# Kernel optimization log

Measured on AMD Instinct MI355X. Metric: run time of the kernel, lower is better.

## Reference

```python
import jax, jax.numpy as jnp
import numpy as np

EPS = 1e-5

def setup_inputs() -> dict:
    key = jax.random.key(0)
    k1, k2 = jax.random.split(key)
    x = jax.random.normal(k1, (4, 2048, 4096), dtype=jnp.float32)
    weight = jax.random.normal(k2, (4096, 4096), dtype=jnp.float32)
    return {"x": x, "weight": weight}

def reference(x, weight):
    # Weight quantization: ternary via absmean scaling.
    delta = jnp.mean(jnp.abs(weight)) + EPS
    w_quant = jnp.clip(jnp.round(weight / delta), -1.0, 1.0)
    w_final = w_quant * delta  # dequantized ternary weights

    # Activation quantization: int8 via per-row absmax.
    gamma = jnp.max(jnp.abs(x), axis=-1, keepdims=True) + EPS
    x_quant = jnp.clip(jnp.round(127.0 * x / gamma), -128.0, 127.0)
    x_quant = (gamma / 127.0) * x_quant
    # NOTE: original forward divides the dequantized activations by gamma
    # again (x_final = x_quant / gamma) -> effectively rounded / 127.
    x_final = x_quant / gamma

    # F.linear(x, W) = x @ W.T
    return jnp.einsum('bsi,oi->bso', x_final, w_final)
```

## Files before the change

### kernel.cpp

```cpp
#include <hip/hip_runtime.h>

#define EPS 1e-5f

typedef int int32x4 __attribute__((ext_vector_type(4)));

typedef const __attribute__((address_space(1))) unsigned int* gaddr_t;
typedef __attribute__((address_space(3))) unsigned int* laddr_t;


__global__ __launch_bounds__(256) void k_abssum(const float* __restrict__ w,
                                                double* __restrict__ partials) {
    int t = threadIdx.x;
    const float4* wv = (const float4*)w + (size_t)blockIdx.x * 4096;
    double s = 0.0;
#pragma unroll
    for (int i = 0; i < 16; ++i) {
        float4 v = wv[i * 256 + t];
        s += (double)(fabsf(v.x) + fabsf(v.y) + fabsf(v.z) + fabsf(v.w));
    }
    for (int off = 32; off; off >>= 1) s += __shfl_down(s, off);
    __shared__ double sm[4];
    int lane = t & 63, wid = t >> 6;
    if (lane == 0) sm[wid] = s;
    __syncthreads();
    if (t == 0) partials[blockIdx.x] = sm[0] + sm[1] + sm[2] + sm[3];
}

__global__ __launch_bounds__(256) void k_delta(const double* __restrict__ partials,
                                               float* __restrict__ delta) {
    int t = threadIdx.x;
    double s = partials[t] + partials[t + 256] + partials[t + 512] + partials[t + 768];
    for (int off = 32; off; off >>= 1) s += __shfl_down(s, off);
    __shared__ double sm[4];
    int lane = t & 63, wid = t >> 6;
    if (lane == 0) sm[wid] = s;
    __syncthreads();
    if (t == 0) {
        double mean = (sm[0] + sm[1] + sm[2] + sm[3]) / 16777216.0;
        *delta = (float)mean + EPS;
    }
}


__global__ __launch_bounds__(256) void k_wquant(const float* __restrict__ w,
                                                const float* __restrict__ deltap,
                                                signed char* __restrict__ tq) {
    float delta = *deltap;
    int t = threadIdx.x;
    size_t b4 = (size_t)blockIdx.x * 4096;
    const float4* wv = (const float4*)w;
    int* qo = (int*)tq;
#pragma unroll
    for (int i = 0; i < 16; ++i) {
        float4 v = wv[b4 + i * 256 + t];
        float a[4] = {v.x, v.y, v.z, v.w};
        int packed = 0;
#pragma unroll
        for (int j = 0; j < 4; ++j) {
            float r = rintf(a[j] / delta);
            r = fminf(1.0f, fmaxf(-1.0f, r));
            packed |= ((int)r & 0xff) << (8 * j);
        }
        qo[b4 + i * 256 + t] = packed;
    }
}

__global__ __launch_bounds__(256) void k_xquant(const float* __restrict__ x,
                                                signed char* __restrict__ q) {
    int t = threadIdx.x;
    size_t rbase = (size_t)blockIdx.x * 4096;
    const float4* xv = (const float4*)(x + rbase);
    float4 v[4];
    float m = 0.0f;
#pragma unroll
    for (int i = 0; i < 4; ++i) {
        v[i] = xv[i * 256 + t];
        m = fmaxf(m, fmaxf(fmaxf(fabsf(v[i].x), fabsf(v[i].y)),
                           fmaxf(fabsf(v[i].z), fabsf(v[i].w))));
    }
    for (int off = 32; off; off >>= 1) m = fmaxf(m, __shfl_xor(m, off));
    __shared__ float wm[4];
    int lane = t & 63, wid = t >> 6;
    if (lane == 0) wm[wid] = m;
    __syncthreads();
    float gamma = fmaxf(fmaxf(wm[0], wm[1]), fmaxf(wm[2], wm[3])) + EPS;
    int* qo = (int*)(q + rbase);
#pragma unroll
    for (int i = 0; i < 4; ++i) {
        float a[4] = {v[i].x, v[i].y, v[i].z, v[i].w};
        int packed = 0;
#pragma unroll
        for (int j = 0; j < 4; ++j) {
            float r = rintf(127.0f * a[j] / gamma);
            r = fminf(127.0f, fmaxf(-128.0f, r));
            packed |= ((int)r & 0xff) << (8 * j);
        }
        qo[i * 256 + t] = packed;
    }
}

__global__ __launch_bounds__(256) void k_gemm(const signed char* __restrict__ A,
                                              const signed char* __restrict__ B,
                                              const float* __restrict__ deltap,
                                              float* __restrict__ C) {
    __shared__ alignas(16) signed char As[8192];
    __shared__ alignas(16) signed char Bs[8192];

    int t = threadIdx.x;
    int lane = t & 63, wid = t >> 6;
    int wr = wid >> 1, wc = wid & 1;

    size_t brow = (size_t)blockIdx.y * 128;
    size_t bcol = (size_t)blockIdx.x * 128;

    int32x4 acc[4][4];
#pragma unroll
    for (int i = 0; i < 4; ++i)
#pragma unroll
        for (int j = 0; j < 4; ++j) acc[i][j] = (int32x4)(0);

    const signed char* ga = A + (brow + (size_t)(wid * 16 + (lane >> 2))) * 4096 + (lane & 3) * 16;
    const signed char* gb = B + (bcol + (size_t)(wid * 16 + (lane >> 2))) * 4096 + (lane & 3) * 16;
    signed char* lA = As + wid * 1024;
    signed char* lB = Bs + wid * 1024;

    int fa_off = (wr * 64 + (lane & 15)) * 64 + (lane >> 4) * 16;
    int fb_off = (wc * 64 + (lane & 15)) * 64 + (lane >> 4) * 16;

    for (int kt = 0; kt < 64; ++kt) {
        int koff = kt * 64;
        __builtin_amdgcn_global_load_lds((gaddr_t)(ga + koff), (laddr_t)lA, 16, 0, 0);
        __builtin_amdgcn_global_load_lds((gaddr_t)(ga + koff + (size_t)64 * 4096),
                                         (laddr_t)(lA + 4096), 16, 0, 0);
        __builtin_amdgcn_global_load_lds((gaddr_t)(gb + koff), (laddr_t)lB, 16, 0, 0);
        __builtin_amdgcn_global_load_lds((gaddr_t)(gb + koff + (size_t)64 * 4096),
                                         (laddr_t)(lB + 4096), 16, 0, 0);
        __syncthreads();

        int32x4 af[4], bf[4];
#pragma unroll
        for (int i = 0; i < 4; ++i)
            af[i] = *(const int32x4*)(As + fa_off + i * 16 * 64);
#pragma unroll
        for (int j = 0; j < 4; ++j)
            bf[j] = *(const int32x4*)(Bs + fb_off + j * 16 * 64);

#pragma unroll
        for (int i = 0; i < 4; ++i)
#pragma unroll
            for (int j = 0; j < 4; ++j)
                acc[i][j] = __builtin_amdgcn_mfma_i32_16x16x64_i8(af[i], bf[j], acc[i][j], 0, 0, 0);
        __syncthreads();
    }

    float scale = (*deltap) / 127.0f;
    size_t orow0 = brow + wr * 64 + (lane >> 4) * 4;
    size_t ocol0 = bcol + wc * 64 + (lane & 15);
#pragma unroll
    for (int i = 0; i < 4; ++i)
#pragma unroll
        for (int j = 0; j < 4; ++j) {
#pragma unroll
            for (int r = 0; r < 4; ++r) {
                C[(orow0 + i * 16 + r) * 4096 + ocol0 + j * 16] =
                    scale * (float)acc[i][j][r];
            }
        }
}


__global__ __launch_bounds__(256) void k_gamma(const float* __restrict__ x,
                                               float* __restrict__ gamma) {
    int t = threadIdx.x;
    size_t rbase = (size_t)blockIdx.x * 4096;
    const float4* xv = (const float4*)(x + rbase);
    float m = 0.0f;
#pragma unroll
    for (int i = 0; i < 4; ++i) {
        float4 v = xv[i * 256 + t];
        m = fmaxf(m, fmaxf(fmaxf(fabsf(v.x), fabsf(v.y)),
                           fmaxf(fabsf(v.z), fabsf(v.w))));
    }
    for (int off = 32; off; off >>= 1) m = fmaxf(m, __shfl_xor(m, off));
    __shared__ float wm[4];
    int lane = t & 63, wid = t >> 6;
    if (lane == 0) wm[wid] = m;
    __syncthreads();
    if (t == 0) gamma[blockIdx.x] = fmaxf(fmaxf(wm[0], wm[1]), fmaxf(wm[2], wm[3])) + EPS;
}

__global__ __launch_bounds__(256) void k_gemm_fb(const float* __restrict__ x,
                                                 const float* __restrict__ w,
                                                 const float* __restrict__ deltap,
                                                 const float* __restrict__ gamma,
                                                 float* __restrict__ C) {
    __shared__ float As[64][33];
    __shared__ float Bs[64][33];
    int t = threadIdx.x;
    int tx = t & 15, ty = t >> 4;
    size_t brow = (size_t)blockIdx.y * 64;
    size_t bcol = (size_t)blockIdx.x * 64;
    float delta = *deltap;
    float rd = 1.0f / delta;
    int lr = t >> 3;
    int lc = (t & 7) * 4;
    float inv0 = 127.0f / gamma[brow + lr];
    float inv1 = 127.0f / gamma[brow + lr + 32];
    float acc[4][4] = {{0.0f}};

    for (int kt = 0; kt < 128; ++kt) {
        int k0 = kt * 32;
#pragma unroll
        for (int h = 0; h < 2; ++h) {
            int row = lr + h * 32;
            float inv = h ? inv1 : inv0;
            float4 v = *(const float4*)(x + (brow + row) * 4096 + k0 + lc);
            As[row][lc + 0] = fminf(127.f, fmaxf(-128.f, rintf(v.x * inv))) * (1.0f / 127.0f);
            As[row][lc + 1] = fminf(127.f, fmaxf(-128.f, rintf(v.y * inv))) * (1.0f / 127.0f);
            As[row][lc + 2] = fminf(127.f, fmaxf(-128.f, rintf(v.z * inv))) * (1.0f / 127.0f);
            As[row][lc + 3] = fminf(127.f, fmaxf(-128.f, rintf(v.w * inv))) * (1.0f / 127.0f);
            float4 u = *(const float4*)(w + (bcol + row) * 4096 + k0 + lc);
            Bs[row][lc + 0] = fminf(1.f, fmaxf(-1.f, rintf(u.x * rd))) * delta;
            Bs[row][lc + 1] = fminf(1.f, fmaxf(-1.f, rintf(u.y * rd))) * delta;
            Bs[row][lc + 2] = fminf(1.f, fmaxf(-1.f, rintf(u.z * rd))) * delta;
            Bs[row][lc + 3] = fminf(1.f, fmaxf(-1.f, rintf(u.w * rd))) * delta;
        }
        __syncthreads();
#pragma unroll 8
        for (int k = 0; k < 32; ++k) {
            float a[4], b[4];
#pragma unroll
            for (int i = 0; i < 4; ++i) { a[i] = As[ty * 4 + i][k]; b[i] = Bs[tx * 4 + i][k]; }
#pragma unroll
            for (int i = 0; i < 4; ++i)
#pragma unroll
                for (int j = 0; j < 4; ++j) acc[i][j] += a[i] * b[j];
        }
        __syncthreads();
    }
#pragma unroll
    for (int i = 0; i < 4; ++i)
#pragma unroll
        for (int j = 0; j < 4; ++j)
            C[(brow + ty * 4 + i) * 4096 + (bcol + tx * 4 + j)] = acc[i][j];
}

extern "C" void kernel_launch(void* const* d_in, const int* in_sizes, int n_in,
                              void* d_out, int out_size, void* d_ws, size_t ws_size,
                              hipStream_t stream) {
    const float* x = (const float*)d_in[0];
    const float* w = (const float*)d_in[1];
    float* out = (float*)d_out;
    char* ws = (char*)d_ws;

    const size_t FULL_WS = 50339848;
    const size_t FB_WS   = 45056;

    if (ws_size >= FULL_WS) {
        signed char* q  = (signed char*)ws;
        signed char* tq = (signed char*)(ws + 33554432);
        double* partials = (double*)(ws + 50331648);
        float* delta = (float*)(ws + 50339840);

        k_abssum<<<1024, 256, 0, stream>>>(w, partials);
        k_delta<<<1, 256, 0, stream>>>(partials, delta);
        k_wquant<<<1024, 256, 0, stream>>>(w, delta, tq);
        k_xquant<<<8192, 256, 0, stream>>>(x, q);
        dim3 grid(32, 64);
        k_gemm<<<grid, 256, 0, stream>>>(q, tq, delta, out);
    } else if (ws_size >= FB_WS) {
        double* partials = (double*)ws;
        float* delta = (float*)(ws + 8192);
        float* gamma = (float*)(ws + 12288);

        k_abssum<<<1024, 256, 0, stream>>>(w, partials);
        k_delta<<<1, 256, 0, stream>>>(partials, delta);
        k_gamma<<<8192, 256, 0, stream>>>(x, gamma);
        dim3 grid(64, 128);
        k_gemm_fb<<<grid, 256, 0, stream>>>(x, w, delta, gamma, out);
    }
}
```

Measured before the change: 429.5 us.

## Remap GEMM workgroups, use wave-per-row activation quant, coarsen weight reduction kernels

The GEMM now remaps its block index so that consecutive workgroups are spread in strides of 8 across the grid, aiming for better L2 locality and XCD-aware placement of A/B tiles. Activation quantization and gamma computation assign one wave per row, which removes shared memory and __syncthreads. The weight abs-sum and ternary quant kernels process more elements per block with fewer blocks, and divisions become multiplications by a precomputed reciprocal. Multiplying by the reciprocal can change rounding at exact ties compared with true division.

```diff
diff --git a/kernel.cpp b/kernel.cpp
--- a/kernel.cpp
+++ b/kernel.cpp
@@ -7,14 +7,13 @@
 typedef const __attribute__((address_space(1))) unsigned int* gaddr_t;
 typedef __attribute__((address_space(3))) unsigned int* laddr_t;
 
-
 __global__ __launch_bounds__(256) void k_abssum(const float* __restrict__ w,
                                                 double* __restrict__ partials) {
     int t = threadIdx.x;
-    const float4* wv = (const float4*)w + (size_t)blockIdx.x * 4096;
+    const float4* wv = (const float4*)w + (size_t)blockIdx.x * 16384;
     double s = 0.0;
-#pragma unroll
-    for (int i = 0; i < 16; ++i) {
+#pragma unroll 8
+    for (int i = 0; i < 64; ++i) {
         float4 v = wv[i * 256 + t];
         s += (double)(fabsf(v.x) + fabsf(v.y) + fabsf(v.z) + fabsf(v.w));
     }
@@ -29,7 +28,7 @@
 __global__ __launch_bounds__(256) void k_delta(const double* __restrict__ partials,
                                                float* __restrict__ delta) {
     int t = threadIdx.x;
-    double s = partials[t] + partials[t + 256] + partials[t + 512] + partials[t + 768];
+    double s = partials[t];
     for (int off = 32; off; off >>= 1) s += __shfl_down(s, off);
     __shared__ double sm[4];
     int lane = t & 63, wid = t >> 6;
@@ -41,23 +40,22 @@
     }
 }
 
-
 __global__ __launch_bounds__(256) void k_wquant(const float* __restrict__ w,
                                                 const float* __restrict__ deltap,
                                                 signed char* __restrict__ tq) {
-    float delta = *deltap;
-    int t = threadIdx.x;
-    size_t b4 = (size_t)blockIdx.x * 4096;
+    float rd = 1.0f / (*deltap);
+    int t = threadIdx.x;
+    size_t b4 = (size_t)blockIdx.x * 8192;
     const float4* wv = (const float4*)w;
     int* qo = (int*)tq;
-#pragma unroll
-    for (int i = 0; i < 16; ++i) {
+#pragma unroll 8
+    for (int i = 0; i < 32; ++i) {
         float4 v = wv[b4 + i * 256 + t];
         float a[4] = {v.x, v.y, v.z, v.w};
         int packed = 0;
 #pragma unroll
         for (int j = 0; j < 4; ++j) {
-            float r = rintf(a[j] / delta);
+            float r = rintf(a[j] * rd);
             r = fminf(1.0f, fmaxf(-1.0f, r));
             packed |= ((int)r & 0xff) << (8 * j);
         }
@@ -68,34 +66,32 @@
 __global__ __launch_bounds__(256) void k_xquant(const float* __restrict__ x,
                                                 signed char* __restrict__ q) {
     int t = threadIdx.x;
-    size_t rbase = (size_t)blockIdx.x * 4096;
-    const float4* xv = (const float4*)(x + rbase);
-    float4 v[4];
+    int lane = t & 63, wid = t >> 6;
+    size_t row = (size_t)blockIdx.x * 4 + wid;
+    const float4* xv = (const float4*)(x + row * 4096);
+    float4 v[16];
     float m = 0.0f;
 #pragma unroll
-    for (int i = 0; i < 4; ++i) {
-        v[i] = xv[i * 256 + t];
+    for (int i = 0; i < 16; ++i) {
+        v[i] = xv[i * 64 + lane];
         m = fmaxf(m, fmaxf(fmaxf(fabsf(v[i].x), fabsf(v[i].y)),
                            fmaxf(fabsf(v[i].z), fabsf(v[i].w))));
     }
+#pragma unroll
     for (int off = 32; off; off >>= 1) m = fmaxf(m, __shfl_xor(m, off));
-    __shared__ float wm[4];
-    int lane = t & 63, wid = t >> 6;
-    if (lane == 0) wm[wid] = m;
-    __syncthreads();
-    float gamma = fmaxf(fmaxf(wm[0], wm[1]), fmaxf(wm[2], wm[3])) + EPS;
-    int* qo = (int*)(q + rbase);
-#pragma unroll
-    for (int i = 0; i < 4; ++i) {
+    float inv = 127.0f / (m + EPS);
+    int* qo = (int*)(q + row * 4096);
+#pragma unroll
+    for (int i = 0; i < 16; ++i) {
         float a[4] = {v[i].x, v[i].y, v[i].z, v[i].w};
         int packed = 0;
 #pragma unroll
         for (int j = 0; j < 4; ++j) {
-            float r = rintf(127.0f * a[j] / gamma);
+            float r = rintf(a[j] * inv);
             r = fminf(127.0f, fmaxf(-128.0f, r));
             packed |= ((int)r & 0xff) << (8 * j);
         }
-        qo[i * 256 + t] = packed;
+        qo[i * 64 + lane] = packed;
     }
 }
 
@@ -110,8 +106,13 @@
     int lane = t & 63, wid = t >> 6;
     int wr = wid >> 1, wc = wid & 1;
 
-    size_t brow = (size_t)blockIdx.y * 128;
-    size_t bcol = (size_t)blockIdx.x * 128;
+    int o = blockIdx.y * 32 + blockIdx.x;
+    int wg = (o & 7) * 256 + (o >> 3);
+    int bx = wg & 31;
+    int by = wg >> 5;
+
+    size_t brow = (size_t)by * 128;
+    size_t bcol = (size_t)bx * 128;
 
     int32x4 acc[4][4];
 #pragma unroll
@@ -172,21 +173,19 @@
 __global__ __launch_bounds__(256) void k_gamma(const float* __restrict__ x,
                                                float* __restrict__ gamma) {
     int t = threadIdx.x;
-    size_t rbase = (size_t)blockIdx.x * 4096;
-    const float4* xv = (const float4*)(x + rbase);
+    int lane = t & 63, wid = t >> 6;
+    size_t row = (size_t)blockIdx.x * 4 + wid;
+    const float4* xv = (const float4*)(x + row * 4096);
     float m = 0.0f;
 #pragma unroll
-    for (int i = 0; i < 4; ++i) {
-        float4 v = xv[i * 256 + t];
+    for (int i = 0; i < 16; ++i) {
+        float4 v = xv[i * 64 + lane];
         m = fmaxf(m, fmaxf(fmaxf(fabsf(v.x), fabsf(v.y)),
                            fmaxf(fabsf(v.z), fabsf(v.w))));
     }
+#pragma unroll
     for (int off = 32; off; off >>= 1) m = fmaxf(m, __shfl_xor(m, off));
-    __shared__ float wm[4];
-    int lane = t & 63, wid = t >> 6;
-    if (lane == 0) wm[wid] = m;
-    __syncthreads();
-    if (t == 0) gamma[blockIdx.x] = fmaxf(fmaxf(wm[0], wm[1]), fmaxf(wm[2], wm[3])) + EPS;
+    if (lane == 0) gamma[row] = m + EPS;
 }
 
 __global__ __launch_bounds__(256) void k_gemm_fb(const float* __restrict__ x,
@@ -262,10 +261,10 @@
         double* partials = (double*)(ws + 50331648);
         float* delta = (float*)(ws + 50339840);
 
-        k_abssum<<<1024, 256, 0, stream>>>(w, partials);
+        k_abssum<<<256, 256, 0, stream>>>(w, partials);
         k_delta<<<1, 256, 0, stream>>>(partials, delta);
-        k_wquant<<<1024, 256, 0, stream>>>(w, delta, tq);
-        k_xquant<<<8192, 256, 0, stream>>>(x, q);
+        k_wquant<<<512, 256, 0, stream>>>(w, delta, tq);
+        k_xquant<<<2048, 256, 0, stream>>>(x, q);
         dim3 grid(32, 64);
         k_gemm<<<grid, 256, 0, stream>>>(q, tq, delta, out);
     } else if (ws_size >= FB_WS) {
@@ -273,9 +272,9 @@
         float* delta = (float*)(ws + 8192);
         float* gamma = (float*)(ws + 12288);
 
-        k_abssum<<<1024, 256, 0, stream>>>(w, partials);
+        k_abssum<<<256, 256, 0, stream>>>(w, partials);
         k_delta<<<1, 256, 0, stream>>>(partials, delta);
-        k_gamma<<<8192, 256, 0, stream>>>(x, gamma);
+        k_gamma<<<2048, 256, 0, stream>>>(x, gamma);
         dim3 grid(64, 128);
         k_gemm_fb<<<grid, 256, 0, stream>>>(x, w, delta, gamma, out);
     }
```

Result: no change. 437.6 us (+1.9%).
